# Kernel tuning notes

Measured on AMD Instinct MI355X. Metric: run time of the kernel, lower is better.

The kernel has to match this reference:

```python
import jax, jax.numpy as jnp
import numpy as np

N_NODES = 100000
N_EDGES = 1600000
D = 64


def setup_inputs() -> dict:
    key = jax.random.key(0)
    k1, k2, k3 = jax.random.split(key, 3)
    x = jax.random.normal(k1, (N_NODES, D), dtype=jnp.float32)
    edge_index = jax.random.randint(k2, (2, N_EDGES), 0, N_NODES, dtype=jnp.int32)
    W = jax.random.normal(k3, (D, D), dtype=jnp.float32) * 0.05  # linear weight [out_dim, in_dim]
    b = jnp.zeros((D,), dtype=jnp.float32)
    return {"x": x, "edge_index": edge_index, "W": W, "b": b}


def reference(x, edge_index, W, b):
    n = x.shape[0]
    # add self loops
    loops = jnp.arange(n, dtype=edge_index.dtype)
    src = jnp.concatenate([edge_index[0], loops])
    dst = jnp.concatenate([edge_index[1], loops])
    # in-degree (counting self loops) via scatter-add of ones onto dst
    deg = jax.ops.segment_sum(jnp.ones_like(src, dtype=x.dtype), dst, num_segments=n)
    deg_inv_sqrt = jnp.where(deg > 0, jax.lax.rsqrt(jnp.maximum(deg, 1.0)) * (deg > 0), 0.0)
    deg_inv_sqrt = jnp.where(deg > 0, deg ** -0.5, 0.0)
    # per-edge symmetric normalization, gather-scale-scatter
    norm = deg_inv_sqrt[src] * deg_inv_sqrt[dst]  # [E+N]
    msgs = x[src] * norm[:, None]                  # [E+N, D] big irregular gather
    out = jax.ops.segment_sum(msgs, dst, num_segments=n)  # scatter-add to nodes
    # dense linear
    return out @ W.T + b
```

## Files before the change

kernel.cpp:

```cpp
#include <hip/hip_runtime.h>


#define BSHIFT 7
#define BNODES 128
#define CAP 3072
#define EPB 4096

typedef short bf16x8 __attribute__((ext_vector_type(8)));
typedef float f32x4 __attribute__((ext_vector_type(4)));

__device__ inline unsigned short f2b_rn(float f) {
    unsigned u = __float_as_uint(f);
    unsigned r = u + 0x7FFFu + ((u >> 16) & 1u);
    return (unsigned short)(r >> 16);
}
__device__ inline float b2f(unsigned short h) {
    return __uint_as_float(((unsigned)h) << 16);
}

__device__ inline void split8(float4 a, float4 b, bf16x8* hi, bf16x8* lo) {
    float f[8] = {a.x, a.y, a.z, a.w, b.x, b.y, b.z, b.w};
    union U { unsigned u[4]; bf16x8 v; } uh, ul;
#pragma unroll
    for (int i = 0; i < 4; ++i) {
        unsigned u0 = __float_as_uint(f[2 * i]);
        unsigned u1 = __float_as_uint(f[2 * i + 1]);
        uh.u[i] = (u0 >> 16) | (u1 & 0xFFFF0000u);
        float r0 = f[2 * i]     - __uint_as_float(u0 & 0xFFFF0000u);
        float r1 = f[2 * i + 1] - __uint_as_float(u1 & 0xFFFF0000u);
        unsigned v0 = __float_as_uint(r0);
        unsigned v1 = __float_as_uint(r1);
        ul.u[i] = (v0 >> 16) | (v1 & 0xFFFF0000u);
    }
    *hi = uh.v;
    *lo = ul.v;
}

__global__ __launch_bounds__(512) void hist_kernel(
    const int* __restrict__ ei, int* __restrict__ h2,
    int e, int G, int nbuck) {
    __shared__ int lh[1024];
    int t = threadIdx.x;
    int g = blockIdx.x;
    for (int i = t; i < nbuck; i += 512) lh[i] = 0;
    __syncthreads();
    int e0 = g * EPB;
    int m = e - e0;
    if (m > EPB) m = EPB;
#pragma unroll
    for (int j = 0; j < 8; ++j) {
        int i = t + j * 512;
        if (i < m) atomicAdd(&lh[ei[e + e0 + i] >> BSHIFT], 1);
    }
    __syncthreads();
    for (int bb = t; bb < nbuck; bb += 512)
        h2[(size_t)g * nbuck + bb] = lh[bb];
}

__global__ __launch_bounds__(64) void scan_kernel(
    const int* __restrict__ h2, int* __restrict__ off2d,
    int* __restrict__ gcur, int G, int nbuck) {
    int bb = blockIdx.x;
    int lane = threadIdx.x;
    int carry = 0;
    int nch = (G + 63) >> 6;
    for (int c = 0; c < nch; ++c) {
        int idx = c * 64 + lane;
        int v = (idx < G) ? h2[(size_t)idx * nbuck + bb] : 0;
        int vi = v;
#pragma unroll
        for (int o = 1; o < 64; o <<= 1) {
            int u = __shfl_up(vi, o, 64);
            if (lane >= o) vi += u;
        }
        if (idx < G) off2d[(size_t)idx * nbuck + bb] = carry + vi - v;
        carry += __shfl(vi, 63, 64);
    }
    if (lane == 0) gcur[bb] = carry;
}

__global__ __launch_bounds__(512) void place_kernel(
    const int* __restrict__ ei, const int* __restrict__ h2,
    const int* __restrict__ off2d, unsigned int* __restrict__ grec,
    int e, int G, int nbuck) {
    __shared__ unsigned int lsort[EPB];
    __shared__ unsigned short sbk[EPB];
    __shared__ int lh[1024];
    __shared__ int lscan[1024];
    __shared__ int goff[1024];
    __shared__ int wsum[8];
    int t = threadIdx.x;
    int g = blockIdx.x;

    for (int bb = t; bb < nbuck; bb += 512) {
        lh[bb] = h2[(size_t)g * nbuck + bb];
        goff[bb] = off2d[(size_t)g * nbuck + bb];
    }
    __syncthreads();

    int b0 = t << 1;
    int v0a = (b0 < nbuck) ? lh[b0] : 0;
    int v1a = (b0 + 1 < nbuck) ? lh[b0 + 1] : 0;
    int ssum = v0a + v1a;
    int lane = t & 63, w = t >> 6;
    int vi = ssum;
#pragma unroll
    for (int o = 1; o < 64; o <<= 1) {
        int u = __shfl_up(vi, o, 64);
        if (lane >= o) vi += u;
    }
    if (lane == 63) wsum[w] = vi;
    __syncthreads();
    int woff = 0;
#pragma unroll
    for (int j = 0; j < 8; ++j)
        if (j < w) woff += wsum[j];
    int ex = woff + vi - ssum;
    if (b0 < nbuck) { lscan[b0] = ex; lh[b0] = 0; }
    if (b0 + 1 < nbuck) { lscan[b0 + 1] = ex + v0a; lh[b0 + 1] = 0; }
    __syncthreads();

    int e0 = g * EPB;
    int m = e - e0;
    if (m > EPB) m = EPB;

#pragma unroll
    for (int j = 0; j < 8; ++j) {
        int i = t + j * 512;
        if (i < m) {
            int gg = e0 + i;
            int s = ei[gg];
            int d = ei[e + gg];
            int b = d >> BSHIFT;
            int sp = lscan[b] + atomicAdd(&lh[b], 1);
            lsort[sp] = ((unsigned int)s << BSHIFT) | (unsigned int)(d & (BNODES - 1));
            sbk[sp] = (unsigned short)b;
        }
    }
    __syncthreads();

#pragma unroll
    for (int j = 0; j < 8; ++j) {
        int i = t + j * 512;
        if (i < m) {
            int b = sbk[i];
            int posb = goff[b] + (i - lscan[b]);
            if (posb < CAP)
                grec[(size_t)b * CAP + posb] = lsort[i];
        }
    }
}

__global__ __launch_bounds__(512) void gemm_scaled_kernel(
    const float* __restrict__ x, const float* __restrict__ W,
    ushort4* __restrict__ yh,
    const unsigned int* __restrict__ grec, const int* __restrict__ gcur,
    int n) {
    __shared__ bf16x8 Whi[512];
    __shared__ bf16x8 Wlo[512];
    __shared__ int lh[BNODES];
    int t = threadIdx.x;
    int b = blockIdx.x;
    int node0 = b << BSHIFT;

    if (t < BNODES) lh[t] = 0;
    __syncthreads();

    size_t base = (size_t)b * CAP;
    int cnt = gcur[b];
    if (cnt > CAP) cnt = CAP;
    for (int i = t; i < cnt; i += 512)
        atomicAdd(&lh[grec[base + i] & (BNODES - 1)], 1);

    {
        int tt = t >> 7, kb = (t >> 6) & 1, g = (t >> 4) & 3, jn = t & 15;
        const float4* wp =
            (const float4*)(W + (size_t)(tt * 16 + jn) * 64 + kb * 32 + g * 8);
        bf16x8 hi, lo;
        split8(wp[0], wp[1], &hi, &lo);
        Whi[t] = hi;
        Wlo[t] = lo;
    }
    __syncthreads();

    int wave = t >> 6, lane = t & 63;
    int jn = lane & 15;
    int g = lane >> 4;
    int node = node0 + wave * 16 + jn;

    bf16x8 xhi[2], xlo[2];
#pragma unroll
    for (int kb = 0; kb < 2; ++kb) {
        float4 p0 = {0.f, 0.f, 0.f, 0.f}, p1 = {0.f, 0.f, 0.f, 0.f};
        if (node < n) {
            const float4* xp =
                (const float4*)(x + (size_t)node * 64 + kb * 32 + g * 8);
            p0 = xp[0];
            p1 = xp[1];
        }
        split8(p0, p1, &xhi[kb], &xlo[kb]);
    }

    float dn = rsqrtf((float)lh[wave * 16 + jn] + 1.0f);

#pragma unroll
    for (int tt = 0; tt < 4; ++tt) {
        f32x4 acc = {0.f, 0.f, 0.f, 0.f};
#pragma unroll
        for (int kb = 0; kb < 2; ++kb) {
            bf16x8 whi = Whi[(tt * 2 + kb) * 64 + lane];
            bf16x8 wlo = Wlo[(tt * 2 + kb) * 64 + lane];
            acc = __builtin_amdgcn_mfma_f32_16x16x32_bf16(wlo, xhi[kb], acc, 0, 0, 0);
            acc = __builtin_amdgcn_mfma_f32_16x16x32_bf16(whi, xlo[kb], acc, 0, 0, 0);
            acc = __builtin_amdgcn_mfma_f32_16x16x32_bf16(whi, xhi[kb], acc, 0, 0, 0);
        }
        if (node < n) {
            ushort4 h;
            h.x = f2b_rn(acc[0] * dn);
            h.y = f2b_rn(acc[1] * dn);
            h.z = f2b_rn(acc[2] * dn);
            h.w = f2b_rn(acc[3] * dn);
            yh[(size_t)node * 16 + (tt * 4 + g)] = h;
        }
    }
}

__global__ __launch_bounds__(512, 4) void csr_gather_kernel(
    const unsigned int* __restrict__ grec, const int* __restrict__ gcur,
    const ushort4* __restrict__ yh, const float* __restrict__ bias,
    float4* __restrict__ out, int n) {
    __shared__ unsigned int sorted[CAP];
    __shared__ int lh[BNODES];
    __shared__ int ls[BNODES + 1];
    __shared__ int wtot;
    int t = threadIdx.x;
    int b = blockIdx.x;
    size_t base = (size_t)b * CAP;
    int cnt = gcur[b];
    if (cnt > CAP) cnt = CAP;
    int node0 = b << BSHIFT;

    if (t < BNODES) lh[t] = 0;
    __syncthreads();
    for (int i = t; i < cnt; i += 512)
        atomicAdd(&lh[grec[base + i] & (BNODES - 1)], 1);
    __syncthreads();
    int c = 0, ex = 0;
    if (t < BNODES) {
        c = lh[t];
        int lane64 = t & 63;
        int v = c;
#pragma unroll
        for (int o = 1; o < 64; o <<= 1) {
            int u = __shfl_up(v, o, 64);
            if (lane64 >= o) v += u;
        }
        if (t == 63) wtot = v;
        ex = v - c;
    }
    __syncthreads();
    if (t >= 64 && t < BNODES) ex += wtot;
    if (t < BNODES) {
        ls[t] = ex;
        lh[t] = 0;
        if (t == BNODES - 1) ls[BNODES] = ex + c;
    }
    __syncthreads();
    for (int i = t; i < cnt; i += 512) {
        unsigned int r = grec[base + i];
        int nd = r & (BNODES - 1);
        int pos = ls[nd] + atomicAdd(&lh[nd], 1);
        sorted[pos] = r >> BSHIFT;
    }
    __syncthreads();

    int wave = t >> 6;
    int lane = t & 63;
    int grp = lane >> 4;
    int fq = lane & 15;
    float4 bb = ((const float4*)bias)[fq];
    for (int i = 0; i < 16; ++i) {
        int nd = wave * 16 + i;
        int node = node0 + nd;
        if (node >= n) break;
        int beg = ls[nd];
        int end = ls[nd + 1];
        float dn = rsqrtf((float)(end - beg) + 1.0f);
        float4 acc = {0.f, 0.f, 0.f, 0.f};
        if (grp == 0) {
            ushort4 h = yh[(size_t)node * 16 + fq];
            acc.x = b2f(h.x); acc.y = b2f(h.y);
            acc.z = b2f(h.z); acc.w = b2f(h.w);
        }
        int j = beg + grp;
        for (; j + 12 < end; j += 16) {
            int s0 = (int)sorted[j];
            int s1 = (int)sorted[j + 4];
            int s2 = (int)sorted[j + 8];
            int s3 = (int)sorted[j + 12];
            ushort4 h0 = yh[(size_t)s0 * 16 + fq];
            ushort4 h1 = yh[(size_t)s1 * 16 + fq];
            ushort4 h2 = yh[(size_t)s2 * 16 + fq];
            ushort4 h3 = yh[(size_t)s3 * 16 + fq];
            acc.x += b2f(h0.x) + b2f(h1.x) + b2f(h2.x) + b2f(h3.x);
            acc.y += b2f(h0.y) + b2f(h1.y) + b2f(h2.y) + b2f(h3.y);
            acc.z += b2f(h0.z) + b2f(h1.z) + b2f(h2.z) + b2f(h3.z);
            acc.w += b2f(h0.w) + b2f(h1.w) + b2f(h2.w) + b2f(h3.w);
        }
        for (; j < end; j += 4) {
            int s = (int)sorted[j];
            ushort4 h = yh[(size_t)s * 16 + fq];
            acc.x += b2f(h.x); acc.y += b2f(h.y);
            acc.z += b2f(h.z); acc.w += b2f(h.w);
        }
        for (int m = 16; m < 64; m <<= 1) {
            acc.x += __shfl_xor(acc.x, m);
            acc.y += __shfl_xor(acc.y, m);
            acc.z += __shfl_xor(acc.z, m);
            acc.w += __shfl_xor(acc.w, m);
        }
        if (lane < 16) {
            float4 o;
            o.x = acc.x * dn + bb.x;
            o.y = acc.y * dn + bb.y;
            o.z = acc.z * dn + bb.z;
            o.w = acc.w * dn + bb.w;
            out[(size_t)node * 16 + lane] = o;
        }
    }
}

extern "C" void kernel_launch(void* const* d_in, const int* in_sizes, int n_in,
                              void* d_out, int out_size, void* d_ws, size_t ws_size,
                              hipStream_t stream) {
    const float* x    = (const float*)d_in[0];
    const int*   ei   = (const int*)d_in[1];
    const float* W    = (const float*)d_in[2];
    const float* bias = (const float*)d_in[3];
    float* out = (float*)d_out;

    int n = in_sizes[0] / 64;
    int e = in_sizes[1] / 2;
    int nbuck = (n + BNODES - 1) / BNODES;
    int G = (e + EPB - 1) / EPB;

    auto align = [](size_t v) { return (v + 255) & ~(size_t)255; };
    char* p = (char*)d_ws;
    int* gcur = (int*)p;                    p += align((size_t)nbuck * 4);
    int* h2 = (int*)p;                      p += align((size_t)G * nbuck * 4);
    int* off2d = (int*)p;                   p += align((size_t)G * nbuck * 4);
    unsigned int* grec = (unsigned int*)p;  p += align((size_t)nbuck * CAP * 4);
    ushort4* yh = (ushort4*)p;

    hist_kernel<<<G, 512, 0, stream>>>(ei, h2, e, G, nbuck);
    scan_kernel<<<nbuck, 64, 0, stream>>>(h2, off2d, gcur, G, nbuck);
    place_kernel<<<G, 512, 0, stream>>>(ei, h2, off2d, grec, e, G, nbuck);
    gemm_scaled_kernel<<<nbuck, 512, 0, stream>>>(x, W, yh, grec, gcur, n);
    csr_gather_kernel<<<nbuck, 512, 0, stream>>>(grec, gcur, yh, bias,
                                                 (float4*)out, n);
}
```

Before: 155.0 us.

## Fuse histogram, scan, placement and GEMM into one persistent kernel with grid barriers

Merges four separate launches (hist, scan, place, scaled GEMM) into a single build kernel that uses atomic-counter grid barriers between phases, with each block handling two buckets for the scan and GEMM phases. This removes three kernel-launch gaps and their serialization overhead. The trade-off is spin-wait barriers that depend on all G blocks being co-resident (G≈391 blocks of 512 threads), a memset launch for the counter, and the deadlock risk that comes with that.

New measurement: 280.3 us. 80.8% more time.

```diff
diff --git a/kernel.cpp b/kernel.cpp
--- a/kernel.cpp
+++ b/kernel.cpp
@@ -36,94 +36,95 @@
     *lo = ul.v;
 }
 
-__global__ __launch_bounds__(512) void hist_kernel(
-    const int* __restrict__ ei, int* __restrict__ h2,
-    int e, int G, int nbuck) {
-    __shared__ int lh[1024];
-    int t = threadIdx.x;
-    int g = blockIdx.x;
-    for (int i = t; i < nbuck; i += 512) lh[i] = 0;
-    __syncthreads();
-    int e0 = g * EPB;
-    int m = e - e0;
-    if (m > EPB) m = EPB;
-#pragma unroll
-    for (int j = 0; j < 8; ++j) {
-        int i = t + j * 512;
-        if (i < m) atomicAdd(&lh[ei[e + e0 + i] >> BSHIFT], 1);
-    }
-    __syncthreads();
-    for (int bb = t; bb < nbuck; bb += 512)
-        h2[(size_t)g * nbuck + bb] = lh[bb];
-}
-
-__global__ __launch_bounds__(64) void scan_kernel(
-    const int* __restrict__ h2, int* __restrict__ off2d,
-    int* __restrict__ gcur, int G, int nbuck) {
-    int bb = blockIdx.x;
-    int lane = threadIdx.x;
-    int carry = 0;
-    int nch = (G + 63) >> 6;
-    for (int c = 0; c < nch; ++c) {
-        int idx = c * 64 + lane;
-        int v = (idx < G) ? h2[(size_t)idx * nbuck + bb] : 0;
-        int vi = v;
-#pragma unroll
-        for (int o = 1; o < 64; o <<= 1) {
-            int u = __shfl_up(vi, o, 64);
-            if (lane >= o) vi += u;
-        }
-        if (idx < G) off2d[(size_t)idx * nbuck + bb] = carry + vi - v;
-        carry += __shfl(vi, 63, 64);
-    }
-    if (lane == 0) gcur[bb] = carry;
-}
-
-__global__ __launch_bounds__(512) void place_kernel(
-    const int* __restrict__ ei, const int* __restrict__ h2,
-    const int* __restrict__ off2d, unsigned int* __restrict__ grec,
-    int e, int G, int nbuck) {
+__device__ inline void gbar(int* cnt, int target) {
+    __syncthreads();
+    if (threadIdx.x == 0) {
+        __threadfence();
+        atomicAdd(cnt, 1);
+        while (atomicAdd(cnt, 0) < target)
+            __builtin_amdgcn_s_sleep(2);
+        __threadfence();
+    }
+    __syncthreads();
+}
+
+__global__ __launch_bounds__(512, 4) void build_kernel(
+    const float* __restrict__ x, const float* __restrict__ W,
+    ushort4* __restrict__ yh, const int* __restrict__ ei,
+    int* __restrict__ h2, int* __restrict__ off2d, int* __restrict__ gcur,
+    unsigned int* __restrict__ grec, int* __restrict__ bar,
+    int n, int e, int G, int nbuck) {
     __shared__ unsigned int lsort[EPB];
     __shared__ unsigned short sbk[EPB];
     __shared__ int lh[1024];
     __shared__ int lscan[1024];
     __shared__ int goff[1024];
     __shared__ int wsum[8];
+    __shared__ bf16x8 Whi[512];
+    __shared__ bf16x8 Wlo[512];
     int t = threadIdx.x;
     int g = blockIdx.x;
-
-    for (int bb = t; bb < nbuck; bb += 512) {
-        lh[bb] = h2[(size_t)g * nbuck + bb];
+    int wave = t >> 6, lane = t & 63;
+
+    for (int i = t; i < nbuck; i += 512) lh[i] = 0;
+    __syncthreads();
+    int e0 = g * EPB;
+    int m = e - e0;
+    if (m > EPB) m = EPB;
+#pragma unroll
+    for (int j = 0; j < 8; ++j) {
+        int i = t + j * 512;
+        if (i < m) atomicAdd(&lh[ei[e + e0 + i] >> BSHIFT], 1);
+    }
+    __syncthreads();
+    for (int bb = t; bb < nbuck; bb += 512)
+        h2[(size_t)g * nbuck + bb] = lh[bb];
+    gbar(bar, G);
+
+    if (wave < 2) {
+        int bb = 2 * g + wave;
+        if (bb < nbuck) {
+            int carry = 0;
+            int nch = (G + 63) >> 6;
+            for (int c = 0; c < nch; ++c) {
+                int idx = c * 64 + lane;
+                int v = (idx < G) ? h2[(size_t)idx * nbuck + bb] : 0;
+                int vi = v;
+#pragma unroll
+                for (int o = 1; o < 64; o <<= 1) {
+                    int u = __shfl_up(vi, o, 64);
+                    if (lane >= o) vi += u;
+                }
+                if (idx < G) off2d[(size_t)idx * nbuck + bb] = carry + vi - v;
+                carry += __shfl(vi, 63, 64);
+            }
+            if (lane == 0) gcur[bb] = carry;
+        }
+    }
+    gbar(bar, 2 * G);
+
+    for (int bb = t; bb < nbuck; bb += 512)
         goff[bb] = off2d[(size_t)g * nbuck + bb];
-    }
-    __syncthreads();
-
     int b0 = t << 1;
     int v0a = (b0 < nbuck) ? lh[b0] : 0;
     int v1a = (b0 + 1 < nbuck) ? lh[b0 + 1] : 0;
     int ssum = v0a + v1a;
-    int lane = t & 63, w = t >> 6;
-    int vi = ssum;
+    int vi2 = ssum;
 #pragma unroll
     for (int o = 1; o < 64; o <<= 1) {
-        int u = __shfl_up(vi, o, 64);
-        if (lane >= o) vi += u;
-    }
-    if (lane == 63) wsum[w] = vi;
+        int u = __shfl_up(vi2, o, 64);
+        if (lane >= o) vi2 += u;
+    }
+    if (lane == 63) wsum[wave] = vi2;
     __syncthreads();
     int woff = 0;
 #pragma unroll
     for (int j = 0; j < 8; ++j)
-        if (j < w) woff += wsum[j];
-    int ex = woff + vi - ssum;
+        if (j < wave) woff += wsum[j];
+    int ex = woff + vi2 - ssum;
     if (b0 < nbuck) { lscan[b0] = ex; lh[b0] = 0; }
     if (b0 + 1 < nbuck) { lscan[b0 + 1] = ex + v0a; lh[b0 + 1] = 0; }
     __syncthreads();
-
-    int e0 = g * EPB;
-    int m = e - e0;
-    if (m > EPB) m = EPB;
-
 #pragma unroll
     for (int j = 0; j < 8; ++j) {
         int i = t + j * 512;
@@ -138,7 +139,6 @@
         }
     }
     __syncthreads();
-
 #pragma unroll
     for (int j = 0; j < 8; ++j) {
         int i = t + j * 512;
@@ -149,78 +149,74 @@
                 grec[(size_t)b * CAP + posb] = lsort[i];
         }
     }
-}
-
-__global__ __launch_bounds__(512) void gemm_scaled_kernel(
-    const float* __restrict__ x, const float* __restrict__ W,
-    ushort4* __restrict__ yh,
-    const unsigned int* __restrict__ grec, const int* __restrict__ gcur,
-    int n) {
-    __shared__ bf16x8 Whi[512];
-    __shared__ bf16x8 Wlo[512];
-    __shared__ int lh[BNODES];
-    int t = threadIdx.x;
-    int b = blockIdx.x;
-    int node0 = b << BSHIFT;
-
-    if (t < BNODES) lh[t] = 0;
-    __syncthreads();
-
-    size_t base = (size_t)b * CAP;
-    int cnt = gcur[b];
-    if (cnt > CAP) cnt = CAP;
-    for (int i = t; i < cnt; i += 512)
-        atomicAdd(&lh[grec[base + i] & (BNODES - 1)], 1);
-
+    gbar(bar, 3 * G);
+
+    if (t < 256) lh[t] = 0;
     {
-        int tt = t >> 7, kb = (t >> 6) & 1, g = (t >> 4) & 3, jn = t & 15;
+        int tt = t >> 7, kb = (t >> 6) & 1, gq = (t >> 4) & 3, jn = t & 15;
         const float4* wp =
-            (const float4*)(W + (size_t)(tt * 16 + jn) * 64 + kb * 32 + g * 8);
+            (const float4*)(W + (size_t)(tt * 16 + jn) * 64 + kb * 32 + gq * 8);
         bf16x8 hi, lo;
         split8(wp[0], wp[1], &hi, &lo);
         Whi[t] = hi;
         Wlo[t] = lo;
     }
     __syncthreads();
-
-    int wave = t >> 6, lane = t & 63;
+#pragma unroll
+    for (int rb = 0; rb < 2; ++rb) {
+        int bk = 2 * g + rb;
+        if (bk < nbuck) {
+            size_t base = (size_t)bk * CAP;
+            int cnt = gcur[bk];
+            if (cnt > CAP) cnt = CAP;
+            for (int i = t; i < cnt; i += 512)
+                atomicAdd(&lh[(rb << 7) + (grec[base + i] & (BNODES - 1))], 1);
+        }
+    }
+    __syncthreads();
+
     int jn = lane & 15;
-    int g = lane >> 4;
-    int node = node0 + wave * 16 + jn;
-
-    bf16x8 xhi[2], xlo[2];
-#pragma unroll
-    for (int kb = 0; kb < 2; ++kb) {
-        float4 p0 = {0.f, 0.f, 0.f, 0.f}, p1 = {0.f, 0.f, 0.f, 0.f};
-        if (node < n) {
-            const float4* xp =
-                (const float4*)(x + (size_t)node * 64 + kb * 32 + g * 8);
-            p0 = xp[0];
-            p1 = xp[1];
-        }
-        split8(p0, p1, &xhi[kb], &xlo[kb]);
-    }
-
-    float dn = rsqrtf((float)lh[wave * 16 + jn] + 1.0f);
-
-#pragma unroll
-    for (int tt = 0; tt < 4; ++tt) {
-        f32x4 acc = {0.f, 0.f, 0.f, 0.f};
+    int gq = lane >> 4;
+#pragma unroll
+    for (int rb = 0; rb < 2; ++rb) {
+        int bk = 2 * g + rb;
+        if (bk >= nbuck) break;
+        int node = (bk << BSHIFT) + wave * 16 + jn;
+
+        bf16x8 xhi[2], xlo[2];
 #pragma unroll
         for (int kb = 0; kb < 2; ++kb) {
-            bf16x8 whi = Whi[(tt * 2 + kb) * 64 + lane];
-            bf16x8 wlo = Wlo[(tt * 2 + kb) * 64 + lane];
-            acc = __builtin_amdgcn_mfma_f32_16x16x32_bf16(wlo, xhi[kb], acc, 0, 0, 0);
-            acc = __builtin_amdgcn_mfma_f32_16x16x32_bf16(whi, xlo[kb], acc, 0, 0, 0);
-            acc = __builtin_amdgcn_mfma_f32_16x16x32_bf16(whi, xhi[kb], acc, 0, 0, 0);
-        }
-        if (node < n) {
-            ushort4 h;
-            h.x = f2b_rn(acc[0] * dn);
-            h.y = f2b_rn(acc[1] * dn);
-            h.z = f2b_rn(acc[2] * dn);
-            h.w = f2b_rn(acc[3] * dn);
-            yh[(size_t)node * 16 + (tt * 4 + g)] = h;
+            float4 p0 = {0.f, 0.f, 0.f, 0.f}, p1 = {0.f, 0.f, 0.f, 0.f};
+            if (node < n) {
+                const float4* xp =
+                    (const float4*)(x + (size_t)node * 64 + kb * 32 + gq * 8);
+                p0 = xp[0];
+                p1 = xp[1];
+            }
+            split8(p0, p1, &xhi[kb], &xlo[kb]);
+        }
+
+        float dn = rsqrtf((float)lh[(rb << 7) + wave * 16 + jn] + 1.0f);
+
+#pragma unroll
+        for (int tt = 0; tt < 4; ++tt) {
+            f32x4 acc = {0.f, 0.f, 0.f, 0.f};
+#pragma unroll
+            for (int kb = 0; kb < 2; ++kb) {
+                bf16x8 whi = Whi[(tt * 2 + kb) * 64 + lane];
+                bf16x8 wlo = Wlo[(tt * 2 + kb) * 64 + lane];
+                acc = __builtin_amdgcn_mfma_f32_16x16x32_bf16(wlo, xhi[kb], acc, 0, 0, 0);
+                acc = __builtin_amdgcn_mfma_f32_16x16x32_bf16(whi, xlo[kb], acc, 0, 0, 0);
+                acc = __builtin_amdgcn_mfma_f32_16x16x32_bf16(whi, xhi[kb], acc, 0, 0, 0);
+            }
+            if (node < n) {
+                ushort4 h;
+                h.x = f2b_rn(acc[0] * dn);
+                h.y = f2b_rn(acc[1] * dn);
+                h.z = f2b_rn(acc[2] * dn);
+                h.w = f2b_rn(acc[3] * dn);
+                yh[(size_t)node * 16 + (tt * 4 + gq)] = h;
+            }
         }
     }
 }
@@ -313,11 +309,11 @@
             acc.x += b2f(h.x); acc.y += b2f(h.y);
             acc.z += b2f(h.z); acc.w += b2f(h.w);
         }
-        for (int m = 16; m < 64; m <<= 1) {
-            acc.x += __shfl_xor(acc.x, m);
-            acc.y += __shfl_xor(acc.y, m);
-            acc.z += __shfl_xor(acc.z, m);
-            acc.w += __shfl_xor(acc.w, m);
+        for (int mm = 16; mm < 64; mm <<= 1) {
+            acc.x += __shfl_xor(acc.x, mm);
+            acc.y += __shfl_xor(acc.y, mm);
+            acc.z += __shfl_xor(acc.z, mm);
+            acc.w += __shfl_xor(acc.w, mm);
         }
         if (lane < 16) {
             float4 o;
@@ -346,16 +342,16 @@
 
     auto align = [](size_t v) { return (v + 255) & ~(size_t)255; };
     char* p = (char*)d_ws;
+    int* bar = (int*)p;                     p += align(4);
     int* gcur = (int*)p;                    p += align((size_t)nbuck * 4);
     int* h2 = (int*)p;                      p += align((size_t)G * nbuck * 4);
     int* off2d = (int*)p;                   p += align((size_t)G * nbuck * 4);
     unsigned int* grec = (unsigned int*)p;  p += align((size_t)nbuck * CAP * 4);
     ushort4* yh = (ushort4*)p;
 
-    hist_kernel<<<G, 512, 0, stream>>>(ei, h2, e, G, nbuck);
-    scan_kernel<<<nbuck, 64, 0, stream>>>(h2, off2d, gcur, G, nbuck);
-    place_kernel<<<G, 512, 0, stream>>>(ei, h2, off2d, grec, e, G, nbuck);
-    gemm_scaled_kernel<<<nbuck, 512, 0, stream>>>(x, W, yh, grec, gcur, n);
+    hipMemsetAsync(bar, 0, 4, stream);
+    build_kernel<<<G, 512, 0, stream>>>(x, W, yh, ei, h2, off2d, gcur, grec,
+                                        bar, n, e, G, nbuck);
     csr_gather_kernel<<<nbuck, 512, 0, stream>>>(grec, gcur, yh, bias,
                                                  (float4*)out, n);
 }
```
